# Performance work log

Hardware: AMD Instinct MI355X
Metric: run time of the kernel (lower is better)

## Reference

```python
import jax, jax.numpy as jnp
import numpy as np

N_NODES = 50000
N_EDGES = 800000
N_GRAPHS = 256
HEADS = 4
OUT_CH = 32
HIDDEN = HEADS * OUT_CH  # 128
NUM_LAYERS = 3
NEG_SLOPE = 0.2
BN_EPS = 1e-5


def setup_inputs() -> dict:
    key = jax.random.key(0)
    ks = jax.random.split(key, 12)
    x = jax.random.normal(ks[0], (N_NODES, HIDDEN), dtype=jnp.float32)
    edge_index = jax.random.randint(ks[1], (2, N_EDGES), 0, N_NODES, dtype=jnp.int64)
    batch = jnp.sort(jax.random.randint(ks[2], (N_NODES,), 0, N_GRAPHS, dtype=jnp.int64))
    s = 1.0 / np.sqrt(HIDDEN)
    W = jax.random.normal(ks[3], (NUM_LAYERS, HIDDEN, HIDDEN), dtype=jnp.float32) * s
    att_src = jax.random.normal(ks[4], (NUM_LAYERS, HEADS, OUT_CH), dtype=jnp.float32) * s
    att_dst = jax.random.normal(ks[5], (NUM_LAYERS, HEADS, OUT_CH), dtype=jnp.float32) * s
    bias = jnp.zeros((NUM_LAYERS, HIDDEN), dtype=jnp.float32)
    bn_gamma = jnp.ones((NUM_LAYERS, HIDDEN), dtype=jnp.float32)
    bn_beta = jnp.zeros((NUM_LAYERS, HIDDEN), dtype=jnp.float32)
    bn_mean = jnp.zeros((NUM_LAYERS, HIDDEN), dtype=jnp.float32)
    bn_var = jnp.ones((NUM_LAYERS, HIDDEN), dtype=jnp.float32)
    fc1_w = jax.random.normal(ks[6], (HIDDEN, HIDDEN // 2), dtype=jnp.float32) * s
    fc1_b = jnp.zeros((HIDDEN // 2,), dtype=jnp.float32)
    fc2_w = jax.random.normal(ks[7], (HIDDEN // 2, 10), dtype=jnp.float32) * (1.0 / np.sqrt(HIDDEN // 2))
    fc2_b = jnp.zeros((10,), dtype=jnp.float32)
    return {"x": x, "edge_index": edge_index, "batch": batch, "W": W,
            "att_src": att_src, "att_dst": att_dst, "bias": bias,
            "bn_gamma": bn_gamma, "bn_beta": bn_beta, "bn_mean": bn_mean,
            "bn_var": bn_var, "fc1_w": fc1_w, "fc1_b": fc1_b,
            "fc2_w": fc2_w, "fc2_b": fc2_b}


def _gat_layer(x, src, dst, W, a_src, a_dst, b):
    n = x.shape[0]
    h = (x @ W).reshape(n, HEADS, OUT_CH)                       # [N,H,C]
    alpha_s = jnp.einsum('nhc,hc->nh', h, a_src)                # [N,H]
    alpha_d = jnp.einsum('nhc,hc->nh', h, a_dst)                # [N,H]
    score = jax.nn.leaky_relu(alpha_s[src] + alpha_d[dst], NEG_SLOPE)  # [E,H]
    # segment softmax over destination node (self-loops guarantee nonempty segments)
    m = jax.lax.stop_gradient(jax.ops.segment_max(score, dst, num_segments=n))
    e = jnp.exp(score - m[dst])
    denom = jax.ops.segment_sum(e, dst, num_segments=n)
    alpha = e / denom[dst]                                      # [E,H]
    msg = h[src] * alpha[:, :, None]                            # [E,H,C]
    out = jax.ops.segment_sum(msg, dst, num_segments=n)         # [N,H,C]
    return out.reshape(n, HEADS * OUT_CH) + b


def reference(x, edge_index, batch, W, att_src, att_dst, bias,
              bn_gamma, bn_beta, bn_mean, bn_var,
              fc1_w, fc1_b, fc2_w, fc2_b):
    n = x.shape[0]
    loop = jnp.arange(n, dtype=edge_index.dtype)
    src = jnp.concatenate([edge_index[0], loop])  # add self-loops (PyG default)
    dst = jnp.concatenate([edge_index[1], loop])
    for i in range(NUM_LAYERS):
        x = _gat_layer(x, src, dst, W[i], att_src[i], att_dst[i], bias[i])
        x = (x - bn_mean[i]) * (bn_gamma[i] / jnp.sqrt(bn_var[i] + BN_EPS)) + bn_beta[i]
        x = jax.nn.elu(x)
    # global mean pool over graphs
    sums = jax.ops.segment_sum(x, batch, num_segments=N_GRAPHS)
    cnts = jax.ops.segment_sum(jnp.ones((n,), dtype=x.dtype), batch, num_segments=N_GRAPHS)
    pooled = sums / jnp.maximum(cnts, 1.0)[:, None]
    hmid = jax.nn.relu(pooled @ fc1_w + fc1_b)
    logits = hmid @ fc2_w + fc2_b
    return logits
```

## Files before the change

kernel.cpp:

```cpp
#include <hip/hip_runtime.h>
#include <hip/hip_fp16.h>
#include <math.h>

#define N_NODES 50000
#define N_EDGES 800000
#define E_TOTAL (N_EDGES + N_NODES)
#define N_GRAPHS 256
#define HEADS 4
#define OUT_CH 32
#define HIDDEN 128
#define NUM_LAYERS 3
#define NEG_SLOPE 0.2f
#define BN_EPS 1e-5f
#define NBLK_SCAN ((N_NODES + 255) / 256)


__global__ void zero_kernel(unsigned int* __restrict__ p, int n) {
    int i = blockIdx.x * blockDim.x + threadIdx.x;
    if (i < n) p[i] = 0u;
}


__global__ void hist_kernel(const int* __restrict__ dst, int* __restrict__ deg,
                            int* __restrict__ rank) {
    int e = blockIdx.x * blockDim.x + threadIdx.x;
    if (e >= E_TOTAL) return;
    int d = (e < N_EDGES) ? dst[e] : (e - N_EDGES);
    rank[e] = atomicAdd(&deg[d], 1);
}

__global__ __launch_bounds__(256) void scan1_kernel(const int* __restrict__ deg,
                                                    int* __restrict__ rowoff,
                                                    int* __restrict__ bsum, int n) {
    int i = blockIdx.x * 256 + threadIdx.x;
    int v = (i < n) ? deg[i] : 0;
    int lane = threadIdx.x & 63, wv = threadIdx.x >> 6;
    int s = v;
    for (int off = 1; off < 64; off <<= 1) {
        int u = __shfl_up(s, off);
        if (lane >= off) s += u;
    }
    __shared__ int wtot[4];
    if (lane == 63) wtot[wv] = s;
    __syncthreads();
    int add = 0;
    for (int w = 0; w < wv; ++w) add += wtot[w];
    s += add;
    if (i < n) rowoff[i + 1] = s;
    if (threadIdx.x == 255) bsum[blockIdx.x] = s;
}

__global__ __launch_bounds__(256) void scan2_kernel(int* __restrict__ bsum, int nb) {
    int t = threadIdx.x;
    int v = (t < nb) ? bsum[t] : 0;
    int lane = t & 63, wv = t >> 6;
    int s = v;
    for (int off = 1; off < 64; off <<= 1) {
        int u = __shfl_up(s, off);
        if (lane >= off) s += u;
    }
    __shared__ int wtot[4];
    if (lane == 63) wtot[wv] = s;
    __syncthreads();
    int add = 0;
    for (int w = 0; w < wv; ++w) add += wtot[w];
    s += add;
    if (t < nb) bsum[t] = s - v;
}

__global__ __launch_bounds__(256) void scan3_kernel(const int* __restrict__ bsum,
                                                    int* __restrict__ rowoff, int n) {
    int i = blockIdx.x * 256 + threadIdx.x;
    if (i == 0) rowoff[0] = 0;
    if (i < n) rowoff[i + 1] += bsum[blockIdx.x];
}

__global__ void scatter_kernel(const int* __restrict__ src, const int* __restrict__ dst,
                               const int* __restrict__ rowoff, const int* __restrict__ rank,
                               int* __restrict__ col) {
    int e = blockIdx.x * blockDim.x + threadIdx.x;
    if (e >= E_TOTAL) return;
    int s, d;
    if (e < N_EDGES) { s = src[e]; d = dst[e]; }
    else             { s = e - N_EDGES; d = s; }
    int pos = rowoff[d] + rank[e];
    col[pos] = s;
}


__global__ __launch_bounds__(256) void gemm_xw(const float* __restrict__ X,
                                               const float* __restrict__ W,
                                               const float* __restrict__ att_src,
                                               const float* __restrict__ att_dst,
                                               __half* __restrict__ Hh,
                                               float* __restrict__ as4,
                                               float* __restrict__ ad4, int n) {
    __shared__ float xst[32][36];
    __shared__ float ws[32][128];
    const int row0 = blockIdx.x * 32;
    const int cg = threadIdx.x & 31;
    const int rg = threadIdx.x >> 5;
    float acc[4][4];
#pragma unroll
    for (int r = 0; r < 4; ++r)
#pragma unroll
        for (int j = 0; j < 4; ++j) acc[r][j] = 0.f;

    for (int k0 = 0; k0 < 128; k0 += 32) {
        {
            int r = threadIdx.x >> 3;
            int kk = (threadIdx.x & 7) * 4;
            int swz = (kk >> 2) & 7;
            int cswz = (((r >> 2) ^ swz) << 2) | (r & 3);
            int gr = row0 + r;
            float4 v = make_float4(0.f, 0.f, 0.f, 0.f);
            if (gr < n) v = *reinterpret_cast<const float4*>(&X[gr * 128 + k0 + kk]);
            xst[kk + 0][cswz] = v.x; xst[kk + 1][cswz] = v.y;
            xst[kk + 2][cswz] = v.z; xst[kk + 3][cswz] = v.w;
        }
        for (int i = threadIdx.x; i < 32 * 128 / 4; i += 256) {
            int p = i * 4;
            int kk = p >> 7, cc = p & 127;
            *reinterpret_cast<float4*>(&ws[kk][cc]) =
                *reinterpret_cast<const float4*>(&W[(k0 + kk) * 128 + cc]);
        }
        __syncthreads();
#pragma unroll
        for (int kk = 0; kk < 32; ++kk) {
            const int swz = (kk >> 2) & 7;
            float4 wv = *reinterpret_cast<const float4*>(&ws[kk][cg * 4]);
            float4 xv = *reinterpret_cast<const float4*>(&xst[kk][((rg ^ swz) << 2)]);
            acc[0][0] += xv.x * wv.x; acc[0][1] += xv.x * wv.y; acc[0][2] += xv.x * wv.z; acc[0][3] += xv.x * wv.w;
            acc[1][0] += xv.y * wv.x; acc[1][1] += xv.y * wv.y; acc[1][2] += xv.y * wv.z; acc[1][3] += xv.y * wv.w;
            acc[2][0] += xv.z * wv.x; acc[2][1] += xv.z * wv.y; acc[2][2] += xv.z * wv.z; acc[2][3] += xv.z * wv.w;
            acc[3][0] += xv.w * wv.x; acc[3][1] += xv.w * wv.y; acc[3][2] += xv.w * wv.z; acc[3][3] += xv.w * wv.w;
        }
        __syncthreads();
    }

#pragma unroll
    for (int r = 0; r < 4; ++r) {
        int gr = row0 + rg * 4 + r;
        if (gr < n) {
            __half2 ab = __floats2half2_rn(acc[r][0], acc[r][1]);
            __half2 cd = __floats2half2_rn(acc[r][2], acc[r][3]);
            uint2 u;
            u.x = *reinterpret_cast<unsigned*>(&ab);
            u.y = *reinterpret_cast<unsigned*>(&cd);
            *reinterpret_cast<uint2*>(&Hh[(size_t)gr * 128 + cg * 4]) = u;
        }
    }

    const int h = cg >> 3;
    const int co = (cg & 7) * 4;
    float4 asw = *reinterpret_cast<const float4*>(att_src + h * OUT_CH + co);
    float4 adw = *reinterpret_cast<const float4*>(att_dst + h * OUT_CH + co);
#pragma unroll
    for (int r = 0; r < 4; ++r) {
        float s = acc[r][0] * asw.x + acc[r][1] * asw.y + acc[r][2] * asw.z + acc[r][3] * asw.w;
        float d = acc[r][0] * adw.x + acc[r][1] * adw.y + acc[r][2] * adw.z + acc[r][3] * adw.w;
        s += __shfl_xor(s, 1); d += __shfl_xor(d, 1);
        s += __shfl_xor(s, 2); d += __shfl_xor(d, 2);
        s += __shfl_xor(s, 4); d += __shfl_xor(d, 4);
        if ((cg & 7) == 0) {
            int gr = row0 + rg * 4 + r;
            if (gr < n) {
                as4[gr * 4 + h] = s;
                ad4[gr * 4 + h] = d;
            }
        }
    }
}


__global__ __launch_bounds__(256) void aggregate_kernel(
    const __half2* __restrict__ Hh2, const float* __restrict__ as4, const float* __restrict__ ad4,
    const int* __restrict__ rowoff, const int* __restrict__ col,
    const float* __restrict__ bias, const float* __restrict__ gamma, const float* __restrict__ beta,
    const float* __restrict__ mean, const float* __restrict__ var,
    float* __restrict__ Xout, int n) {
    __shared__ float4 esc_s[4][64];
    int wid = (blockIdx.x * blockDim.x + threadIdx.x) >> 6;
    if (wid >= n) return;
    int lane = threadIdx.x & 63;
    int wv = (threadIdx.x >> 6) & 3;
    int hd = lane >> 4;
    int c = lane * 2;

    float4 adv4 = *reinterpret_cast<const float4*>(&ad4[wid * 4]);
    const float* escp = reinterpret_cast<const float*>(&esc_s[wv][0]);

    int jbeg = rowoff[wid], jend = rowoff[wid + 1];

    float s = 0.f, ax = 0.f, ay = 0.f;

    for (int base = jbeg; base < jend; base += 64) {
        int myj = base + lane;
        int mysrc = (myj < jend) ? col[myj] : 0;
        int cnt = min(64, jend - base);

        {
            float4 a = *reinterpret_cast<const float4*>(&as4[mysrc * 4]);
            float x0 = a.x + adv4.x; x0 = x0 > 0.f ? x0 : x0 * NEG_SLOPE;
            float x1 = a.y + adv4.y; x1 = x1 > 0.f ? x1 : x1 * NEG_SLOPE;
            float x2 = a.z + adv4.z; x2 = x2 > 0.f ? x2 : x2 * NEG_SLOPE;
            float x3 = a.w + adv4.w; x3 = x3 > 0.f ? x3 : x3 * NEG_SLOPE;
            esc_s[wv][lane] = make_float4(__expf(x0), __expf(x1), __expf(x2), __expf(x3));
        }

        int t = 0;
#pragma unroll 1
        for (; t + 8 <= cnt; t += 8) {
            int s0 = __shfl(mysrc, t + 0);
            int s1 = __shfl(mysrc, t + 1);
            int s2 = __shfl(mysrc, t + 2);
            int s3 = __shfl(mysrc, t + 3);
            int s4 = __shfl(mysrc, t + 4);
            int s5 = __shfl(mysrc, t + 5);
            int s6 = __shfl(mysrc, t + 6);
            int s7 = __shfl(mysrc, t + 7);
            float e0 = escp[(t + 0) * 4 + hd];
            float e1 = escp[(t + 1) * 4 + hd];
            float e2 = escp[(t + 2) * 4 + hd];
            float e3 = escp[(t + 3) * 4 + hd];
            float e4 = escp[(t + 4) * 4 + hd];
            float e5 = escp[(t + 5) * 4 + hd];
            float e6 = escp[(t + 6) * 4 + hd];
            float e7 = escp[(t + 7) * 4 + hd];
            float2 h0 = __half22float2(Hh2[(size_t)s0 * 64 + lane]);
            float2 h1 = __half22float2(Hh2[(size_t)s1 * 64 + lane]);
            float2 h2 = __half22float2(Hh2[(size_t)s2 * 64 + lane]);
            float2 h3 = __half22float2(Hh2[(size_t)s3 * 64 + lane]);
            float2 h4 = __half22float2(Hh2[(size_t)s4 * 64 + lane]);
            float2 h5 = __half22float2(Hh2[(size_t)s5 * 64 + lane]);
            float2 h6 = __half22float2(Hh2[(size_t)s6 * 64 + lane]);
            float2 h7 = __half22float2(Hh2[(size_t)s7 * 64 + lane]);
            s  += ((e0 + e1) + (e2 + e3)) + ((e4 + e5) + (e6 + e7));
            ax += e0 * h0.x + e1 * h1.x + e2 * h2.x + e3 * h3.x
                + e4 * h4.x + e5 * h5.x + e6 * h6.x + e7 * h7.x;
            ay += e0 * h0.y + e1 * h1.y + e2 * h2.y + e3 * h3.y
                + e4 * h4.y + e5 * h5.y + e6 * h6.y + e7 * h7.y;
        }
        for (; t < cnt; ++t) {
            int src = __shfl(mysrc, t);
            float e = escp[t * 4 + hd];
            float2 hv = __half22float2(Hh2[(size_t)src * 64 + lane]);
            s += e;
            ax += e * hv.x;
            ay += e * hv.y;
        }
    }

    float inv = 1.f / s;
    float v0 = ax * inv + bias[c];
    float v1 = ay * inv + bias[c + 1];
    v0 = (v0 - mean[c])     * (gamma[c]     * rsqrtf(var[c]     + BN_EPS)) + beta[c];
    v1 = (v1 - mean[c + 1]) * (gamma[c + 1] * rsqrtf(var[c + 1] + BN_EPS)) + beta[c + 1];
    v0 = v0 > 0.f ? v0 : expm1f(v0);
    v1 = v1 > 0.f ? v1 : expm1f(v1);
    float2 o = make_float2(v0, v1);
    *reinterpret_cast<float2*>(&Xout[(size_t)wid * HIDDEN + c]) = o;
}


__global__ __launch_bounds__(1024) void pool_fc_kernel(
    const float* __restrict__ X, const int* __restrict__ batch,
    const float* __restrict__ fc1w, const float* __restrict__ fc1b,
    const float* __restrict__ fc2w, const float* __restrict__ fc2b,
    float* __restrict__ out) {
    int g = blockIdx.x;
    int tid = threadIdx.x;
    int cg = (tid & 31) * 4;
    int rg = tid >> 5;

    int lo = 0, hi = N_NODES;
    while (lo < hi) { int mid = (lo + hi) >> 1; if (batch[mid] < g) lo = mid + 1; else hi = mid; }
    int lo2 = lo, hi2 = N_NODES;
    while (lo2 < hi2) { int mid = (lo2 + hi2) >> 1; if (batch[mid] < g + 1) lo2 = mid + 1; else hi2 = mid; }

    float ax = 0.f, ay = 0.f, az = 0.f, aw = 0.f;
    for (int i = lo + rg; i < lo2; i += 32) {
        float4 v = *reinterpret_cast<const float4*>(&X[(size_t)i * HIDDEN + cg]);
        ax += v.x; ay += v.y; az += v.z; aw += v.w;
    }

    __shared__ float red[32][132];
    red[rg][cg + 0] = ax; red[rg][cg + 1] = ay;
    red[rg][cg + 2] = az; red[rg][cg + 3] = aw;
    __syncthreads();
#pragma unroll
    for (int step = 16; step >= 1; step >>= 1) {
        if (rg < step) {
            red[rg][cg + 0] += red[rg + step][cg + 0];
            red[rg][cg + 1] += red[rg + step][cg + 1];
            red[rg][cg + 2] += red[rg + step][cg + 2];
            red[rg][cg + 3] += red[rg + step][cg + 3];
        }
        __syncthreads();
    }

    __shared__ float pooled[HIDDEN];
    __shared__ float hmid[64];
    if (rg == 0) {
        float inv = 1.f / fmaxf((float)(lo2 - lo), 1.0f);
        pooled[cg + 0] = red[0][cg + 0] * inv;
        pooled[cg + 1] = red[0][cg + 1] * inv;
        pooled[cg + 2] = red[0][cg + 2] * inv;
        pooled[cg + 3] = red[0][cg + 3] * inv;
    }
    __syncthreads();
    if (tid < 64) {
        float a = fc1b[tid];
#pragma unroll 8
        for (int k = 0; k < 128; ++k) a += pooled[k] * fc1w[k * 64 + tid];
        hmid[tid] = fmaxf(a, 0.f);
    }
    __syncthreads();
    if (tid < 10) {
        float a = fc2b[tid];
#pragma unroll 8
        for (int k = 0; k < 64; ++k) a += hmid[k] * fc2w[k * 10 + tid];
        out[g * 10 + tid] = a;
    }
}


static inline size_t align_up(size_t x, size_t a) { return (x + a - 1) & ~(a - 1); }

extern "C" void kernel_launch(void* const* d_in, const int* in_sizes, int n_in,
                              void* d_out, int out_size, void* d_ws, size_t ws_size,
                              hipStream_t stream) {
    const float* x        = (const float*)d_in[0];
    const int*   eidx     = (const int*)d_in[1];
    const int*   batch    = (const int*)d_in[2];
    const float* W        = (const float*)d_in[3];
    const float* att_src  = (const float*)d_in[4];
    const float* att_dst  = (const float*)d_in[5];
    const float* bias     = (const float*)d_in[6];
    const float* bn_gamma = (const float*)d_in[7];
    const float* bn_beta  = (const float*)d_in[8];
    const float* bn_mean  = (const float*)d_in[9];
    const float* bn_var   = (const float*)d_in[10];
    const float* fc1w     = (const float*)d_in[11];
    const float* fc1b     = (const float*)d_in[12];
    const float* fc2w     = (const float*)d_in[13];
    const float* fc2b     = (const float*)d_in[14];
    float* out = (float*)d_out;

    const int* src = eidx;
    const int* dst = eidx + N_EDGES;

    char* p = (char*)d_ws;
    size_t off = 0;
    auto alloc = [&](size_t bytes) {
        size_t o = off;
        off = align_up(off + bytes, 256);
        return (void*)(p + o);
    };
    __half* Hh     = (__half*)alloc((size_t)N_NODES * HIDDEN * 2);
    float* Xbuf    = (float*)alloc((size_t)N_NODES * HIDDEN * 4);
    float* as4     = (float*)alloc((size_t)N_NODES * HEADS * 4);
    float* ad4     = (float*)alloc((size_t)N_NODES * HEADS * 4);
    int*   deg     = (int*)alloc((size_t)N_NODES * 4);
    int*   rowoff  = (int*)alloc((size_t)(N_NODES + 1) * 4);
    int*   rank    = (int*)alloc((size_t)E_TOTAL * 4);
    int*   bsum    = (int*)alloc((size_t)NBLK_SCAN * 4);
    int*   col     = (int*)alloc((size_t)E_TOTAL * 4);
    (void)n_in; (void)in_sizes; (void)out_size; (void)ws_size;

    zero_kernel<<<(N_NODES + 255) / 256, 256, 0, stream>>>((unsigned int*)deg, N_NODES);

    hist_kernel<<<(E_TOTAL + 255) / 256, 256, 0, stream>>>(dst, deg, rank);
    scan1_kernel<<<NBLK_SCAN, 256, 0, stream>>>(deg, rowoff, bsum, N_NODES);
    scan2_kernel<<<1, 256, 0, stream>>>(bsum, NBLK_SCAN);
    scan3_kernel<<<NBLK_SCAN, 256, 0, stream>>>(bsum, rowoff, N_NODES);
    scatter_kernel<<<(E_TOTAL + 255) / 256, 256, 0, stream>>>(src, dst, rowoff, rank, col);

    const float* xcur = x;
    for (int layer = 0; layer < NUM_LAYERS; ++layer) {
        const float* Wl  = W + (size_t)layer * HIDDEN * HIDDEN;
        const float* asl = att_src + (size_t)layer * HEADS * OUT_CH;
        const float* adl = att_dst + (size_t)layer * HEADS * OUT_CH;
        const float* bl  = bias + (size_t)layer * HIDDEN;
        const float* gl  = bn_gamma + (size_t)layer * HIDDEN;
        const float* btl = bn_beta + (size_t)layer * HIDDEN;
        const float* ml  = bn_mean + (size_t)layer * HIDDEN;
        const float* vl  = bn_var + (size_t)layer * HIDDEN;

        gemm_xw<<<(N_NODES + 31) / 32, 256, 0, stream>>>(xcur, Wl, asl, adl, Hh, as4, ad4, N_NODES);
        aggregate_kernel<<<(N_NODES * 64 + 255) / 256, 256, 0, stream>>>(
            (const __half2*)Hh, as4, ad4, rowoff, col, bl, gl, btl, ml, vl, Xbuf, N_NODES);
        xcur = Xbuf;
    }

    pool_fc_kernel<<<N_GRAPHS, 1024, 0, stream>>>(xcur, batch, fc1w, fc1b, fc2w, fc2b, out);
}
```

Measured before the change: 383.7 us.

## Use fp16 MFMA for XW GEMM and scalar-load neighbor indices in aggregation

Replaces the LDS-tiled fp32 FMA GEMM with direct-from-global fp16 MFMA 16x16x32 tiles, each wave owning one head's 32 columns. The attention dot products are then reduced with 16-lane shuffles. In the aggregation kernel, neighbor indices are read as wave-uniform scalar loads from col instead of cross-lane shuffles. The aim is to cut GEMM ALU and LDS cost and shuffle latency. In exchange, X and W are quantized to fp16 before the multiply, W is read uncoalesced and strided, and the Hh stores are scalar.

Measured after the change: 372.8 us. 2.8% less time.

```diff
diff --git a/kernel.cpp b/kernel.cpp
--- a/kernel.cpp
+++ b/kernel.cpp
@@ -14,6 +14,9 @@
 #define BN_EPS 1e-5f
 #define NBLK_SCAN ((N_NODES + 255) / 256)
 
+typedef _Float16 half8v __attribute__((ext_vector_type(8)));
+typedef float float4v __attribute__((ext_vector_type(4)));
+
 
 __global__ void zero_kernel(unsigned int* __restrict__ p, int n) {
     int i = blockIdx.x * blockDim.x + threadIdx.x;
@@ -95,81 +98,87 @@
                                                __half* __restrict__ Hh,
                                                float* __restrict__ as4,
                                                float* __restrict__ ad4, int n) {
-    __shared__ float xst[32][36];
-    __shared__ float ws[32][128];
     const int row0 = blockIdx.x * 32;
-    const int cg = threadIdx.x & 31;
-    const int rg = threadIdx.x >> 5;
-    float acc[4][4];
-#pragma unroll
-    for (int r = 0; r < 4; ++r)
-#pragma unroll
-        for (int j = 0; j < 4; ++j) acc[r][j] = 0.f;
-
+    const int lane = threadIdx.x & 63;
+    const int w = threadIdx.x >> 6;
+    const int cw = w * 32;
+    const int r16 = lane & 15;
+    const int g = lane >> 4;
+
+    float4v acc[2][2];
+#pragma unroll
+    for (int m = 0; m < 2; ++m)
+#pragma unroll
+        for (int ct = 0; ct < 2; ++ct)
+#pragma unroll
+            for (int i = 0; i < 4; ++i) acc[m][ct][i] = 0.f;
+
+#pragma unroll
     for (int k0 = 0; k0 < 128; k0 += 32) {
-        {
-            int r = threadIdx.x >> 3;
-            int kk = (threadIdx.x & 7) * 4;
-            int swz = (kk >> 2) & 7;
-            int cswz = (((r >> 2) ^ swz) << 2) | (r & 3);
-            int gr = row0 + r;
-            float4 v = make_float4(0.f, 0.f, 0.f, 0.f);
-            if (gr < n) v = *reinterpret_cast<const float4*>(&X[gr * 128 + k0 + kk]);
-            xst[kk + 0][cswz] = v.x; xst[kk + 1][cswz] = v.y;
-            xst[kk + 2][cswz] = v.z; xst[kk + 3][cswz] = v.w;
-        }
-        for (int i = threadIdx.x; i < 32 * 128 / 4; i += 256) {
-            int p = i * 4;
-            int kk = p >> 7, cc = p & 127;
-            *reinterpret_cast<float4*>(&ws[kk][cc]) =
-                *reinterpret_cast<const float4*>(&W[(k0 + kk) * 128 + cc]);
-        }
-        __syncthreads();
-#pragma unroll
-        for (int kk = 0; kk < 32; ++kk) {
-            const int swz = (kk >> 2) & 7;
-            float4 wv = *reinterpret_cast<const float4*>(&ws[kk][cg * 4]);
-            float4 xv = *reinterpret_cast<const float4*>(&xst[kk][((rg ^ swz) << 2)]);
-            acc[0][0] += xv.x * wv.x; acc[0][1] += xv.x * wv.y; acc[0][2] += xv.x * wv.z; acc[0][3] += xv.x * wv.w;
-            acc[1][0] += xv.y * wv.x; acc[1][1] += xv.y * wv.y; acc[1][2] += xv.y * wv.z; acc[1][3] += xv.y * wv.w;
-            acc[2][0] += xv.z * wv.x; acc[2][1] += xv.z * wv.y; acc[2][2] += xv.z * wv.z; acc[2][3] += xv.z * wv.w;
-            acc[3][0] += xv.w * wv.x; acc[3][1] += xv.w * wv.y; acc[3][2] += xv.w * wv.z; acc[3][3] += xv.w * wv.w;
-        }
-        __syncthreads();
-    }
-
-#pragma unroll
-    for (int r = 0; r < 4; ++r) {
-        int gr = row0 + rg * 4 + r;
-        if (gr < n) {
-            __half2 ab = __floats2half2_rn(acc[r][0], acc[r][1]);
-            __half2 cd = __floats2half2_rn(acc[r][2], acc[r][3]);
-            uint2 u;
-            u.x = *reinterpret_cast<unsigned*>(&ab);
-            u.y = *reinterpret_cast<unsigned*>(&cd);
-            *reinterpret_cast<uint2*>(&Hh[(size_t)gr * 128 + cg * 4]) = u;
-        }
-    }
-
-    const int h = cg >> 3;
-    const int co = (cg & 7) * 4;
-    float4 asw = *reinterpret_cast<const float4*>(att_src + h * OUT_CH + co);
-    float4 adw = *reinterpret_cast<const float4*>(att_dst + h * OUT_CH + co);
-#pragma unroll
-    for (int r = 0; r < 4; ++r) {
-        float s = acc[r][0] * asw.x + acc[r][1] * asw.y + acc[r][2] * asw.z + acc[r][3] * asw.w;
-        float d = acc[r][0] * adw.x + acc[r][1] * adw.y + acc[r][2] * adw.z + acc[r][3] * adw.w;
-        s += __shfl_xor(s, 1); d += __shfl_xor(d, 1);
-        s += __shfl_xor(s, 2); d += __shfl_xor(d, 2);
-        s += __shfl_xor(s, 4); d += __shfl_xor(d, 4);
-        if ((cg & 7) == 0) {
-            int gr = row0 + rg * 4 + r;
+        const int kk = k0 + g * 8;
+        half8v a[2], b[2];
+#pragma unroll
+        for (int m = 0; m < 2; ++m) {
+            int gr = row0 + m * 16 + r16;
+            float4 x0 = make_float4(0.f, 0.f, 0.f, 0.f);
+            float4 x1 = make_float4(0.f, 0.f, 0.f, 0.f);
             if (gr < n) {
-                as4[gr * 4 + h] = s;
-                ad4[gr * 4 + h] = d;
+                const float* xp = &X[(size_t)gr * 128 + kk];
+                x0 = *reinterpret_cast<const float4*>(xp);
+                x1 = *reinterpret_cast<const float4*>(xp + 4);
             }
-        }
-    }
+            a[m][0] = (_Float16)x0.x; a[m][1] = (_Float16)x0.y;
+            a[m][2] = (_Float16)x0.z; a[m][3] = (_Float16)x0.w;
+            a[m][4] = (_Float16)x1.x; a[m][5] = (_Float16)x1.y;
+            a[m][6] = (_Float16)x1.z; a[m][7] = (_Float16)x1.w;
+        }
+#pragma unroll
+        for (int ct = 0; ct < 2; ++ct) {
+            const float* wp = &W[(size_t)kk * 128 + cw + ct * 16 + r16];
+#pragma unroll
+            for (int j = 0; j < 8; ++j) b[ct][j] = (_Float16)wp[(size_t)j * 128];
+        }
+#pragma unroll
+        for (int m = 0; m < 2; ++m)
+#pragma unroll
+            for (int ct = 0; ct < 2; ++ct)
+                acc[m][ct] = __builtin_amdgcn_mfma_f32_16x16x32_f16(a[m], b[ct], acc[m][ct], 0, 0, 0);
+    }
+
+#pragma unroll
+    for (int m = 0; m < 2; ++m)
+#pragma unroll
+        for (int i = 0; i < 4; ++i) {
+            int gr = row0 + m * 16 + g * 4 + i;
+            if (gr < n) {
+#pragma unroll
+                for (int ct = 0; ct < 2; ++ct)
+                    Hh[(size_t)gr * 128 + cw + ct * 16 + r16] = (__half)acc[m][ct][i];
+            }
+        }
+
+    float asw0 = att_src[cw + r16];
+    float asw1 = att_src[cw + 16 + r16];
+    float adw0 = att_dst[cw + r16];
+    float adw1 = att_dst[cw + 16 + r16];
+#pragma unroll
+    for (int m = 0; m < 2; ++m)
+#pragma unroll
+        for (int i = 0; i < 4; ++i) {
+            float s = acc[m][0][i] * asw0 + acc[m][1][i] * asw1;
+            float d = acc[m][0][i] * adw0 + acc[m][1][i] * adw1;
+            s += __shfl_xor(s, 1); d += __shfl_xor(d, 1);
+            s += __shfl_xor(s, 2); d += __shfl_xor(d, 2);
+            s += __shfl_xor(s, 4); d += __shfl_xor(d, 4);
+            s += __shfl_xor(s, 8); d += __shfl_xor(d, 8);
+            if (r16 == 0) {
+                int gr = row0 + m * 16 + g * 4 + i;
+                if (gr < n) {
+                    as4[gr * 4 + w] = s;
+                    ad4[gr * 4 + w] = d;
+                }
+            }
+        }
 }
 
 
@@ -198,6 +207,8 @@
         int myj = base + lane;
         int mysrc = (myj < jend) ? col[myj] : 0;
         int cnt = min(64, jend - base);
+        int bu = __builtin_amdgcn_readfirstlane(base);
+        const int* cu = col + bu;
 
         {
             float4 a = *reinterpret_cast<const float4*>(&as4[mysrc * 4]);
@@ -211,14 +222,14 @@
         int t = 0;
 #pragma unroll 1
         for (; t + 8 <= cnt; t += 8) {
-            int s0 = __shfl(mysrc, t + 0);
-            int s1 = __shfl(mysrc, t + 1);
-            int s2 = __shfl(mysrc, t + 2);
-            int s3 = __shfl(mysrc, t + 3);
-            int s4 = __shfl(mysrc, t + 4);
-            int s5 = __shfl(mysrc, t + 5);
-            int s6 = __shfl(mysrc, t + 6);
-            int s7 = __shfl(mysrc, t + 7);
+            int s0 = cu[t + 0];
+            int s1 = cu[t + 1];
+            int s2 = cu[t + 2];
+            int s3 = cu[t + 3];
+            int s4 = cu[t + 4];
+            int s5 = cu[t + 5];
+            int s6 = cu[t + 6];
+            int s7 = cu[t + 7];
             float e0 = escp[(t + 0) * 4 + hd];
             float e1 = escp[(t + 1) * 4 + hd];
             float e2 = escp[(t + 2) * 4 + hd];
@@ -242,7 +253,7 @@
                 + e4 * h4.y + e5 * h5.y + e6 * h6.y + e7 * h7.y;
         }
         for (; t < cnt; ++t) {
-            int src = __shfl(mysrc, t);
+            int src = cu[t];
             float e = escp[t * 4 + hd];
             float2 hv = __half22float2(Hh2[(size_t)src * 64 + lane]);
             s += e;
```
